# Optimization experiments

Hardware: AMD Instinct MI355X
Metric: run time of the kernel (lower is better)

The kernel has to match this reference:

```python
import jax, jax.numpy as jnp
import numpy as np

ETA_MIN = 0.02
ETA_MAX = 0.35
RHO = 0.001
NEG_INF = -1e6


def _build_transition(boundary_probs, K):
    # boundary_probs: (B, T) in [0,1]
    eta = jnp.clip(ETA_MIN + (ETA_MAX - ETA_MIN) * boundary_probs, 0.001, 0.95)  # (B,T)
    B, T = eta.shape
    dtype = eta.dtype
    idx = jnp.arange(K)
    # diagonal: row0 -> 1-eta, last row -> 1-rho, middle -> clamp(1-eta-rho, 0.01)
    stay_mid = jnp.maximum(1.0 - eta - RHO, 0.01)
    diag = jnp.broadcast_to(stay_mid[..., None], (B, T, K))
    diag = diag.at[..., 0].set(1.0 - eta)
    diag = diag.at[..., K - 1].set(1.0 - RHO)
    A = jnp.zeros((B, T, K, K), dtype=dtype)
    A = A.at[..., idx, idx].set(diag)
    # superdiagonal (rows 0..K-2): advance prob eta
    A = A.at[..., idx[:-1], idx[:-1] + 1].set(jnp.broadcast_to(eta[..., None], (B, T, K - 1)))
    # subdiagonal (rows 1..K-1): backtrack prob rho
    A = A.at[..., idx[1:], idx[1:] - 1].set(RHO)
    A = A / jnp.clip(A.sum(axis=-1, keepdims=True), 1e-8)
    return A


def setup_inputs() -> dict:
    key = jax.random.key(0)
    k1, k2 = jax.random.split(key)
    B, T, K = 32, 4096, 16
    emission_log_probs = jax.random.normal(k1, (B, T, K), dtype=jnp.float32)
    boundary_probs = jax.random.uniform(k2, (B, T), dtype=jnp.float32)
    mask = jnp.ones((B, T), dtype=jnp.float32)
    return {"emission_log_probs": emission_log_probs,
            "boundary_probs": boundary_probs,
            "mask": mask}


def reference(emission_log_probs, boundary_probs, mask):
    B, T, K = emission_log_probs.shape
    dtype = emission_log_probs.dtype
    A = _build_transition(boundary_probs, K)          # (B,T,K,K)
    log_A = jnp.log(jnp.clip(A, 1e-10))               # (B,T,K,K)

    log_alpha0 = jnp.full((B, K), NEG_INF, dtype=dtype).at[:, 0].set(0.0)

    # t = 0 (no transition)
    lj0 = log_alpha0 + emission_log_probs[:, 0]
    lZ0 = jax.nn.logsumexp(lj0, axis=-1, keepdims=True)
    la0_new = lj0 - lZ0
    m0 = mask[:, 0][:, None]
    la0 = m0 * la0_new + (1.0 - m0) * log_alpha0
    lZ0_out = mask[:, 0] * lZ0[:, 0]

    def step(log_alpha, inp):
        lA_t, em_t, m_t = inp                          # (B,K,K), (B,K), (B,)
        # logsumexp over previous-state axis i: lA_t[b,i,j] + log_alpha[b,i]
        pred = jax.nn.logsumexp(lA_t + log_alpha[:, :, None], axis=1)
        lj = pred + em_t
        lZ = jax.nn.logsumexp(lj, axis=-1, keepdims=True)
        new = lj - lZ
        m = m_t[:, None]
        log_alpha = m * new + (1.0 - m) * log_alpha
        return log_alpha, (log_alpha, m_t * lZ[:, 0])

    xs = (jnp.moveaxis(log_A, 1, 0)[1:],
          jnp.moveaxis(emission_log_probs, 1, 0)[1:],
          jnp.moveaxis(mask, 1, 0)[1:])
    _, (las, lZs) = jax.lax.scan(step, la0, xs)

    log_beliefs = jnp.moveaxis(jnp.concatenate([la0[None], las], axis=0), 0, 1)  # (B,T,K)
    log_normalizers = jnp.moveaxis(jnp.concatenate([lZ0_out[None], lZs], axis=0), 0, 1)  # (B,T)
    beliefs = jnp.exp(log_beliefs)
    return beliefs, log_beliefs, log_normalizers, A
```

## Files before the change

### kernel.cpp

```cpp
#include <hip/hip_runtime.h>


#define BB 32
#define TT 4096
#define KK 16
#define LCH 64
#define NCH 64

constexpr float RHO  = 0.001f;
constexpr float LEAK = 1e-10f;

template<int CTRL>
__device__ __forceinline__ float dppf(float x) {
  return __uint_as_float((unsigned)__builtin_amdgcn_update_dpp(
      0, (int)__float_as_uint(x), CTRL, 0xF, 0xF, true));
}
__device__ __forceinline__ float sum16(float x) {
  x += dppf<0xB1>(x);
  x += dppf<0x4E>(x);
  x += dppf<0x141>(x);
  x += dppf<0x140>(x);
  return x;
}
__device__ __forceinline__ float rdfirst(float x) {
  return __uint_as_float((unsigned)__builtin_amdgcn_readfirstlane((int)__float_as_uint(x)));
}

struct Coefs { float cL, cD, cR, E; };

__device__ __forceinline__ Coefs make_coefs(int j, float bpt, float emt) {
  float eta = fminf(fmaxf(fmaf(0.33f, bpt, 0.02f), 0.001f), 0.95f);
  float dm  = fmaxf((1.0f - eta) - RHO, 0.01f);
  float s0  = (1.0f - eta) + eta;
  float sm  = (RHO + dm) + eta;
  float s15 = RHO + (1.0f - RHO);
  float i0  = __builtin_amdgcn_rcpf(s0);
  float im  = __builtin_amdgcn_rcpf(sm);
  float i15 = __builtin_amdgcn_rcpf(s15);
  float i_jm1 = (j == 1) ? i0 : im;
  float i_j   = (j == 0) ? i0 : ((j == 15) ? i15 : im);
  float i_jp1 = (j == 14) ? i15 : im;
  float diag  = (j == 0) ? (1.0f - eta) : ((j == 15) ? (1.0f - RHO) : dm);
  Coefs c;
  c.cL = fmaf(eta,  i_jm1, -LEAK);
  c.cD = fmaf(diag, i_j,   -LEAK);
  c.cR = fmaf(RHO,  i_jp1, -LEAK);
  c.E  = __expf(emt);
  return c;
}

__global__ __launch_bounds__(256) void phase1_kernel(
    const float* __restrict__ em, const float* __restrict__ bp,
    const float* __restrict__ msk, float* __restrict__ Gbuf)
{
  int wid  = blockIdx.x * 4 + (threadIdx.x >> 6);
  int lane = threadIdx.x & 63;
  int g = lane >> 4, j = lane & 15;
  int b = wid & 31;
  int c = wid >> 5;
  long t0 = (long)c * LCH + 1;
  const float* emb = em  + ((long)b * TT + t0) * KK;
  const float* bpb = bp  + (long)b * TT + t0;
  const float* mb  = msk + (long)b * TT + t0;

  float r0 = (j == 4*g + 0) ? 1.0f : 0.0f;
  float r1 = (j == 4*g + 1) ? 1.0f : 0.0f;
  float r2 = (j == 4*g + 2) ? 1.0f : 0.0f;
  float r3 = (j == 4*g + 3) ? 1.0f : 0.0f;

  float em_c = emb[j], bp_c = bpb[0], m_c = mb[0];
  for (int s = 0; s < LCH; ++s) {
    int sn = (s + 1 < LCH) ? s + 1 : s;
    float em_n = emb[(long)sn * KK + j];
    float bp_n = bpb[sn];
    float m_n  = mb[sn];

    Coefs cf = make_coefs(j, bp_c, em_c);
    bool on  = (m_c != 0.0f);
    float cL = on ? cf.cL : 0.0f;
    float cD = on ? cf.cD : 1.0f;
    float cR = on ? cf.cR : 0.0f;
    float lk = on ? LEAK  : 0.0f;
    float E  = on ? cf.E  : 1.0f;

    float S0 = sum16(r0), S1 = sum16(r1), S2 = sum16(r2), S3 = sum16(r3);
    float part = (S0 + S1) + (S2 + S3);
    part += __shfl_xor(part, 16);
    part += __shfl_xor(part, 32);
    float Es = E * __builtin_amdgcn_rcpf(part);

    float pl0 = dppf<0x111>(r0), pr0 = dppf<0x101>(r0);
    float pl1 = dppf<0x111>(r1), pr1 = dppf<0x101>(r1);
    float pl2 = dppf<0x111>(r2), pr2 = dppf<0x101>(r2);
    float pl3 = dppf<0x111>(r3), pr3 = dppf<0x101>(r3);
    r0 = Es * fmaf(pl0, cL, fmaf(r0, cD, fmaf(pr0, cR, lk * S0)));
    r1 = Es * fmaf(pl1, cL, fmaf(r1, cD, fmaf(pr1, cR, lk * S1)));
    r2 = Es * fmaf(pl2, cL, fmaf(r2, cD, fmaf(pr2, cR, lk * S2)));
    r3 = Es * fmaf(pl3, cL, fmaf(r3, cD, fmaf(pr3, cR, lk * S3)));

    em_c = em_n; bp_c = bp_n; m_c = m_n;
  }
  float4 v; v.x = r0; v.y = r1; v.z = r2; v.w = r3;
  ((float4*)(Gbuf + ((long)(b * NCH + c) << 8)))[j * 4 + g] = v;
}

__global__ __launch_bounds__(256) void phase2_kernel(
    const float* __restrict__ em, const float* __restrict__ msk,
    const float* __restrict__ Gbuf, float* __restrict__ Pst)
{
  int b    = blockIdx.x * 4 + (threadIdx.x >> 6);
  int lane = threadIdx.x & 63;
  int g = lane >> 4, j = lane & 15;

  float em0  = em[(long)b * TT * KK + j];
  float em00 = rdfirst(em0);
  float m0   = msk[(long)b * TT];
  float la_init = (j == 0) ? 0.0f : -1000000.0f;
  float la0 = m0 * ((la_init + em0) - em00) + (1.0f - m0) * la_init;
  float P   = __expf(la0);

  const int src = 20 * g;
  float4 grow = *((const float4*)(Gbuf + ((long)(b * NCH) << 8)) + (j * 4 + g));
  for (int c = 0; c < NCH; ++c) {
    if (lane < 16) Pst[((long)(b * NCH + c) << 4) + j] = P;
    if (c == NCH - 1) break;
    float4 gnext = grow;
    if (c + 1 < NCH - 1)
      gnext = *((const float4*)(Gbuf + ((long)(b * NCH + c + 1) << 8)) + (j * 4 + g));
    float p0 = __shfl(P, src + 0), p1 = __shfl(P, src + 1);
    float p2 = __shfl(P, src + 2), p3 = __shfl(P, src + 3);
    float up = grow.x * p0;
    up = fmaf(grow.y, p1, up);
    up = fmaf(grow.z, p2, up);
    up = fmaf(grow.w, p3, up);
    up += __shfl_xor(up, 16);
    up += __shfl_xor(up, 32);
    float S = sum16(up);
    P = up * __builtin_amdgcn_rcpf(S);
    grow = gnext;
  }
}

__global__ __launch_bounds__(256) void phase3_kernel(
    const float* __restrict__ em, const float* __restrict__ bp,
    const float* __restrict__ msk, const float* __restrict__ Pst,
    float* __restrict__ out)
{
  const long BTK = (long)BB * TT * KK;
  float* beliefs = out;
  float* logb    = out + BTK;
  float* lzs     = out + 2 * BTK;

  int wid  = blockIdx.x * 4 + (threadIdx.x >> 6);
  int lane = threadIdx.x & 63;
  int j = lane & 15;
  int b = wid & 31;
  int c = wid >> 5;

  const float* emb = em  + (long)b * TT * KK;
  const float* bpb = bp  + (long)b * TT;
  const float* mb  = msk + (long)b * TT;
  float* belb = beliefs + (long)b * TT * KK;
  float* lbb  = logb    + (long)b * TT * KK;
  float* lzb  = lzs     + (long)b * TT;

  float P = Pst[((long)(b * NCH + c) << 4) + j];

  if (c == 0) {
    float em0  = emb[j];
    float em00 = rdfirst(em0);
    float m0   = mb[0];
    float la_init = (j == 0) ? 0.0f : -1000000.0f;
    float la0 = m0 * ((la_init + em0) - em00) + (1.0f - m0) * la_init;
    if (lane < 16) {
      belb[j] = P;
      lbb[j]  = la0;
      if (j == 0) lzb[0] = m0 * em00;
    }
  }

  int t0 = c * LCH + 1;
  int t1 = (t0 + LCH - 1 < TT - 1) ? (t0 + LCH - 1) : (TT - 1);

  float em_c = emb[(long)t0 * KK + j], bp_c = bpb[t0], m_c = mb[t0];
  for (int t = t0; t <= t1; ++t) {
    int tn = (t + 1 <= t1) ? t + 1 : t;
    float em_n = emb[(long)tn * KK + j];
    float bp_n = bpb[tn];
    float m_n  = mb[tn];

    Coefs cf = make_coefs(j, bp_c, em_c);
    float pl = dppf<0x111>(P), pr = dppf<0x101>(P);
    float pred = fmaf(pl, cf.cL, fmaf(P, cf.cD, fmaf(pr, cf.cR, LEAK)));
    float u = pred * cf.E;
    float S = sum16(u);
    float Pn = u * __builtin_amdgcn_rcpf(S);
    bool on = (m_c != 0.0f);
    P = on ? Pn : P;
    if (lane < 16) {
      belb[(long)t * KK + j] = P;
      lbb[(long)t * KK + j]  = __logf(P);
      if (j == 0) lzb[t] = on ? __logf(S) : 0.0f;
    }
    em_c = em_n; bp_c = bp_n; m_c = m_n;
  }
}

__global__ __launch_bounds__(256) void a_writer_kernel(
    const float* __restrict__ bp, float* __restrict__ Aout)
{
  long tid  = (long)blockIdx.x * 256 + threadIdx.x;
  long flat = tid * 4;
  int  bt   = (int)(flat >> 8);
  int  rem  = (int)(flat & 255);
  int  r    = rem >> 4;
  int  c0   = rem & 15;
  float p   = bp[bt];
  float eta = fminf(fmaxf(0.02f + 0.33f * p, 0.001f), 0.95f);
  float diag, s;
  if (r == 0)       { diag = 1.0f - eta; s = (1.0f - eta) + eta; }
  else if (r == 15) { diag = 1.0f - RHO; s = RHO + (1.0f - RHO); }
  else { diag = fmaxf((1.0f - eta) - RHO, 0.01f); s = (RHO + diag) + eta; }
  s = fmaxf(s, 1e-8f);
  float inv = 1.0f / s;
  float4 v;
  float* vp = &v.x;
  #pragma unroll
  for (int q = 0; q < 4; ++q) {
    int cc = c0 + q;
    float a = (cc == r) ? diag : (cc == r + 1) ? eta : (cc == r - 1) ? RHO : 0.0f;
    vp[q] = a * inv;
  }
  ((float4*)Aout)[tid] = v;
}

extern "C" void kernel_launch(void* const* d_in, const int* in_sizes, int n_in,
                              void* d_out, int out_size, void* d_ws, size_t ws_size,
                              hipStream_t stream) {
  const float* em = (const float*)d_in[0];
  const float* bp = (const float*)d_in[1];
  const float* mk = (const float*)d_in[2];
  float* out = (float*)d_out;

  const long BTK = (long)BB * TT * KK;
  float* Gbuf = out;
  float* Aout = out + 2 * BTK + (long)BB * TT;
  float* Pst  = Aout;

  hipLaunchKernelGGL(phase1_kernel, dim3(504),   dim3(256), 0, stream, em, bp, mk, Gbuf);
  hipLaunchKernelGGL(phase2_kernel, dim3(8),     dim3(256), 0, stream, em, mk, Gbuf, Pst);
  hipLaunchKernelGGL(phase3_kernel, dim3(512),   dim3(256), 0, stream, em, bp, mk, Pst, out);
  hipLaunchKernelGGL(a_writer_kernel, dim3(32768), dim3(256), 0, stream, bp, Aout);
}
```

Measured before the change: 238.8 us.

## Batch phase1 normalization every 4 steps and pack 4 chunks per wave in phase3

Phase1 now renormalizes the 16x16 propagator only once every four steps, dropping the leak term. It also unrolls by four with a prefetched input batch, which removes per-step cross-lane reductions from the serial chain. Phase3 maps four chunks onto the four 16-lane rows of each wavefront instead of leaving 48 lanes idle, so it needs only 128 blocks. The risk is fewer waves in phase3 to hide latency, and small numerical drift in the phase1 propagator because the leak term is dropped and normalization is deferred.

```diff
diff --git a/kernel.cpp b/kernel.cpp
--- a/kernel.cpp
+++ b/kernel.cpp
@@ -24,29 +24,6 @@
 }
 __device__ __forceinline__ float rdfirst(float x) {
   return __uint_as_float((unsigned)__builtin_amdgcn_readfirstlane((int)__float_as_uint(x)));
-}
-
-struct Coefs { float cL, cD, cR, E; };
-
-__device__ __forceinline__ Coefs make_coefs(int j, float bpt, float emt) {
-  float eta = fminf(fmaxf(fmaf(0.33f, bpt, 0.02f), 0.001f), 0.95f);
-  float dm  = fmaxf((1.0f - eta) - RHO, 0.01f);
-  float s0  = (1.0f - eta) + eta;
-  float sm  = (RHO + dm) + eta;
-  float s15 = RHO + (1.0f - RHO);
-  float i0  = __builtin_amdgcn_rcpf(s0);
-  float im  = __builtin_amdgcn_rcpf(sm);
-  float i15 = __builtin_amdgcn_rcpf(s15);
-  float i_jm1 = (j == 1) ? i0 : im;
-  float i_j   = (j == 0) ? i0 : ((j == 15) ? i15 : im);
-  float i_jp1 = (j == 14) ? i15 : im;
-  float diag  = (j == 0) ? (1.0f - eta) : ((j == 15) ? (1.0f - RHO) : dm);
-  Coefs c;
-  c.cL = fmaf(eta,  i_jm1, -LEAK);
-  c.cD = fmaf(diag, i_j,   -LEAK);
-  c.cR = fmaf(RHO,  i_jp1, -LEAK);
-  c.E  = __expf(emt);
-  return c;
 }
 
 __global__ __launch_bounds__(256) void phase1_kernel(
@@ -68,37 +45,52 @@
   float r2 = (j == 4*g + 2) ? 1.0f : 0.0f;
   float r3 = (j == 4*g + 3) ? 1.0f : 0.0f;
 
-  float em_c = emb[j], bp_c = bpb[0], m_c = mb[0];
-  for (int s = 0; s < LCH; ++s) {
-    int sn = (s + 1 < LCH) ? s + 1 : s;
-    float em_n = emb[(long)sn * KK + j];
-    float bp_n = bpb[sn];
-    float m_n  = mb[sn];
-
-    Coefs cf = make_coefs(j, bp_c, em_c);
-    bool on  = (m_c != 0.0f);
-    float cL = on ? cf.cL : 0.0f;
-    float cD = on ? cf.cD : 1.0f;
-    float cR = on ? cf.cR : 0.0f;
-    float lk = on ? LEAK  : 0.0f;
-    float E  = on ? cf.E  : 1.0f;
-
-    float S0 = sum16(r0), S1 = sum16(r1), S2 = sum16(r2), S3 = sum16(r3);
-    float part = (S0 + S1) + (S2 + S3);
-    part += __shfl_xor(part, 16);
-    part += __shfl_xor(part, 32);
-    float Es = E * __builtin_amdgcn_rcpf(part);
-
-    float pl0 = dppf<0x111>(r0), pr0 = dppf<0x101>(r0);
-    float pl1 = dppf<0x111>(r1), pr1 = dppf<0x101>(r1);
-    float pl2 = dppf<0x111>(r2), pr2 = dppf<0x101>(r2);
-    float pl3 = dppf<0x111>(r3), pr3 = dppf<0x101>(r3);
-    r0 = Es * fmaf(pl0, cL, fmaf(r0, cD, fmaf(pr0, cR, lk * S0)));
-    r1 = Es * fmaf(pl1, cL, fmaf(r1, cD, fmaf(pr1, cR, lk * S1)));
-    r2 = Es * fmaf(pl2, cL, fmaf(r2, cD, fmaf(pr2, cR, lk * S2)));
-    r3 = Es * fmaf(pl3, cL, fmaf(r3, cD, fmaf(pr3, cR, lk * S3)));
-
-    em_c = em_n; bp_c = bp_n; m_c = m_n;
+  float emv[4], bpv[4], mv[4];
+  #pragma unroll
+  for (int k = 0; k < 4; ++k) {
+    emv[k] = emb[(long)k * KK + j]; bpv[k] = bpb[k]; mv[k] = mb[k];
+  }
+  for (int s0 = 0; s0 < LCH; s0 += 4) {
+    float emn[4], bpn[4], mn[4];
+    #pragma unroll
+    for (int k = 0; k < 4; ++k) {
+      int sn = s0 + 4 + k; if (sn > LCH - 1) sn = LCH - 1;
+      emn[k] = emb[(long)sn * KK + j]; bpn[k] = bpb[sn]; mn[k] = mb[sn];
+    }
+    #pragma unroll
+    for (int k = 0; k < 4; ++k) {
+      float eta = fminf(fmaxf(fmaf(0.33f, bpv[k], 0.02f), 0.001f), 0.95f);
+      float dm  = fmaxf((1.0f - eta) - RHO, 0.01f);
+      float s0n = (1.0f - eta) + eta;
+      float smn = (RHO + dm) + eta;
+      float i0  = __builtin_amdgcn_rcpf(s0n);
+      float im  = __builtin_amdgcn_rcpf(smn);
+      float i_jm1 = (j == 1) ? i0 : im;
+      float i_j   = (j == 0) ? i0 : ((j == 15) ? 1.0f : im);
+      float i_jp1 = (j == 14) ? 1.0f : im;
+      float diag  = (j == 0) ? (1.0f - eta) : ((j == 15) ? (1.0f - RHO) : dm);
+      bool on  = (mv[k] != 0.0f);
+      float cL = on ? eta  * i_jm1 : 0.0f;
+      float cD = on ? diag * i_j   : 1.0f;
+      float cR = on ? RHO  * i_jp1 : 0.0f;
+      float E  = on ? __expf(emv[k]) : 1.0f;
+
+      float pl0 = dppf<0x111>(r0), pr0 = dppf<0x101>(r0);
+      float pl1 = dppf<0x111>(r1), pr1 = dppf<0x101>(r1);
+      float pl2 = dppf<0x111>(r2), pr2 = dppf<0x101>(r2);
+      float pl3 = dppf<0x111>(r3), pr3 = dppf<0x101>(r3);
+      r0 = E * fmaf(pl0, cL, fmaf(r0, cD, pr0 * cR));
+      r1 = E * fmaf(pl1, cL, fmaf(r1, cD, pr1 * cR));
+      r2 = E * fmaf(pl2, cL, fmaf(r2, cD, pr2 * cR));
+      r3 = E * fmaf(pl3, cL, fmaf(r3, cD, pr3 * cR));
+    }
+    float grand = sum16((r0 + r1) + (r2 + r3));
+    grand += __shfl_xor(grand, 16);
+    grand += __shfl_xor(grand, 32);
+    float sc = __builtin_amdgcn_rcpf(grand);
+    r0 *= sc; r1 *= sc; r2 *= sc; r3 *= sc;
+    #pragma unroll
+    for (int k = 0; k < 4; ++k) { emv[k] = emn[k]; bpv[k] = bpn[k]; mv[k] = mn[k]; }
   }
   float4 v; v.x = r0; v.y = r1; v.z = r2; v.w = r3;
   ((float4*)(Gbuf + ((long)(b * NCH + c) << 8)))[j * 4 + g] = v;
@@ -153,9 +145,10 @@
 
   int wid  = blockIdx.x * 4 + (threadIdx.x >> 6);
   int lane = threadIdx.x & 63;
-  int j = lane & 15;
-  int b = wid & 31;
-  int c = wid >> 5;
+  int j   = lane & 15;
+  int row = lane >> 4;
+  int b   = wid >> 4;
+  int c   = ((wid & 15) << 2) + row;
 
   const float* emb = em  + (long)b * TT * KK;
   const float* bpb = bp  + (long)b * TT;
@@ -172,37 +165,58 @@
     float m0   = mb[0];
     float la_init = (j == 0) ? 0.0f : -1000000.0f;
     float la0 = m0 * ((la_init + em0) - em00) + (1.0f - m0) * la_init;
-    if (lane < 16) {
-      belb[j] = P;
-      lbb[j]  = la0;
-      if (j == 0) lzb[0] = m0 * em00;
-    }
-  }
-
-  int t0 = c * LCH + 1;
-  int t1 = (t0 + LCH - 1 < TT - 1) ? (t0 + LCH - 1) : (TT - 1);
-
-  float em_c = emb[(long)t0 * KK + j], bp_c = bpb[t0], m_c = mb[t0];
-  for (int t = t0; t <= t1; ++t) {
-    int tn = (t + 1 <= t1) ? t + 1 : t;
-    float em_n = emb[(long)tn * KK + j];
-    float bp_n = bpb[tn];
-    float m_n  = mb[tn];
-
-    Coefs cf = make_coefs(j, bp_c, em_c);
-    float pl = dppf<0x111>(P), pr = dppf<0x101>(P);
-    float pred = fmaf(pl, cf.cL, fmaf(P, cf.cD, fmaf(pr, cf.cR, LEAK)));
-    float u = pred * cf.E;
-    float S = sum16(u);
-    float Pn = u * __builtin_amdgcn_rcpf(S);
-    bool on = (m_c != 0.0f);
-    P = on ? Pn : P;
-    if (lane < 16) {
-      belb[(long)t * KK + j] = P;
-      lbb[(long)t * KK + j]  = __logf(P);
-      if (j == 0) lzb[t] = on ? __logf(S) : 0.0f;
-    }
-    em_c = em_n; bp_c = bp_n; m_c = m_n;
+    belb[j] = P;
+    lbb[j]  = la0;
+    if (j == 0) lzb[0] = m0 * em00;
+  }
+
+  const int t0 = (c << 6) + 1;
+  float emv[4], bpv[4], mv[4];
+  #pragma unroll
+  for (int k = 0; k < 4; ++k) {
+    int ts = t0 + k; if (ts > TT - 1) ts = TT - 1;
+    emv[k] = emb[(long)ts * KK + j]; bpv[k] = bpb[ts]; mv[k] = mb[ts];
+  }
+  for (int i0 = 0; i0 < LCH; i0 += 4) {
+    float emn[4], bpn[4], mn[4];
+    #pragma unroll
+    for (int k = 0; k < 4; ++k) {
+      int ts = t0 + i0 + 4 + k; if (ts > TT - 1) ts = TT - 1;
+      emn[k] = emb[(long)ts * KK + j]; bpn[k] = bpb[ts]; mn[k] = mb[ts];
+    }
+    #pragma unroll
+    for (int k = 0; k < 4; ++k) {
+      int t = t0 + i0 + k;
+      float eta = fminf(fmaxf(fmaf(0.33f, bpv[k], 0.02f), 0.001f), 0.95f);
+      float dm  = fmaxf((1.0f - eta) - RHO, 0.01f);
+      float s0n = (1.0f - eta) + eta;
+      float smn = (RHO + dm) + eta;
+      float i0r = __builtin_amdgcn_rcpf(s0n);
+      float im  = __builtin_amdgcn_rcpf(smn);
+      float i_jm1 = (j == 1) ? i0r : im;
+      float i_j   = (j == 0) ? i0r : ((j == 15) ? 1.0f : im);
+      float i_jp1 = (j == 14) ? 1.0f : im;
+      float diag  = (j == 0) ? (1.0f - eta) : ((j == 15) ? (1.0f - RHO) : dm);
+      float cL = fmaf(eta,  i_jm1, -LEAK);
+      float cD = fmaf(diag, i_j,   -LEAK);
+      float cR = fmaf(RHO,  i_jp1, -LEAK);
+      float E  = __expf(emv[k]);
+
+      float pl = dppf<0x111>(P), pr = dppf<0x101>(P);
+      float pred = fmaf(pl, cL, fmaf(P, cD, fmaf(pr, cR, LEAK)));
+      float u = pred * E;
+      float S = sum16(u);
+      float Pn = u * __builtin_amdgcn_rcpf(S);
+      bool on = (mv[k] != 0.0f);
+      if (t < TT) {
+        P = on ? Pn : P;
+        belb[(long)t * KK + j] = P;
+        lbb[(long)t * KK + j]  = __logf(P);
+        if (j == 0) lzb[t] = on ? __logf(S) : 0.0f;
+      }
+    }
+    #pragma unroll
+    for (int k = 0; k < 4; ++k) { emv[k] = emn[k]; bpv[k] = bpn[k]; mv[k] = mn[k]; }
   }
 }
 
@@ -247,8 +261,8 @@
   float* Aout = out + 2 * BTK + (long)BB * TT;
   float* Pst  = Aout;
 
-  hipLaunchKernelGGL(phase1_kernel, dim3(504),   dim3(256), 0, stream, em, bp, mk, Gbuf);
-  hipLaunchKernelGGL(phase2_kernel, dim3(8),     dim3(256), 0, stream, em, mk, Gbuf, Pst);
-  hipLaunchKernelGGL(phase3_kernel, dim3(512),   dim3(256), 0, stream, em, bp, mk, Pst, out);
+  hipLaunchKernelGGL(phase1_kernel,   dim3(504),   dim3(256), 0, stream, em, bp, mk, Gbuf);
+  hipLaunchKernelGGL(phase2_kernel,   dim3(8),     dim3(256), 0, stream, em, mk, Gbuf, Pst);
+  hipLaunchKernelGGL(phase3_kernel,   dim3(128),   dim3(256), 0, stream, em, bp, mk, Pst, out);
   hipLaunchKernelGGL(a_writer_kernel, dim3(32768), dim3(256), 0, stream, bp, Aout);
 }
```

New measurement: 205.6 us. -13.9%, faster.
